# Performance work log

Measured on AMD Instinct MI355X. Metric: run time of the kernel, lower is better.

## Reference

```python
import jax, jax.numpy as jnp
import numpy as np

B, S, IN, OUT = 4, 2048, 4096, 16384

def setup_inputs() -> dict:
    key = jax.random.key(0)
    k1, k2, k3, k4 = jax.random.split(key, 4)
    x = jax.random.normal(k1, (B, S, IN), dtype=jnp.float32)
    quantized_weight = jax.random.randint(k2, (OUT, IN), 0, 16, dtype=jnp.int32)
    scale = jax.random.uniform(k3, (OUT,), dtype=jnp.float32)
    zero_point = jax.random.randint(k4, (OUT,), 0, 16, dtype=jnp.int32)
    return {"x": x, "quantized_weight": quantized_weight, "scale": scale, "zero_point": zero_point}

def reference(x, quantized_weight, scale, zero_point):
    # Per-output-channel dequantization: W = (q - zp) * scale, shape [OUT, IN]
    weight = (quantized_weight.astype(jnp.float32) - zero_point.astype(jnp.float32)[:, None]) * scale[:, None]
    # F.linear(x, W) = x @ W.T -> [B, S, OUT]
    return jnp.einsum('bsi,oi->bso', x, weight)
```

## Files before the change

kernel.cpp:

```cpp
#include <hip/hip_runtime.h>
#include <stdint.h>

#define MDIM 8192
#define NDIM 16384
#define KDIM 4096
#define NT   64

typedef __attribute__((ext_vector_type(4))) int i32x4;

__device__ __forceinline__ void gload_lds16(const void* g, void* l) {
    __builtin_amdgcn_global_load_lds(
        (const __attribute__((address_space(1))) void*)g,
        (__attribute__((address_space(3))) void*)l,
        16, 0, 0);
}

__device__ __forceinline__ i32x4 MFMA8(i32x4 a, i32x4 b, i32x4 c) {
    return __builtin_amdgcn_mfma_i32_16x16x64_i8(a, b, c, 0, 0, 0);
}


__global__ __launch_bounds__(256)
void quant_x_kernel(const float* __restrict__ x, int8_t* __restrict__ xq,
                    float* __restrict__ sx) {
    const int row = (int)blockIdx.x;
    const float* xr = x + (long)row * KDIM;
    const int t = threadIdx.x;
    float v[16];
#pragma unroll
    for (int i = 0; i < 4; ++i)
        *(float4*)&v[i * 4] = ((const float4*)xr)[t + 256 * i];
    float m = 0.f;
#pragma unroll
    for (int i = 0; i < 16; ++i) m = fmaxf(m, fabsf(v[i]));
#pragma unroll
    for (int off = 32; off >= 1; off >>= 1) m = fmaxf(m, __shfl_xor(m, off));
    __shared__ float red[4];
    if ((t & 63) == 0) red[t >> 6] = m;
    __syncthreads();
    m = fmaxf(fmaxf(red[0], red[1]), fmaxf(red[2], red[3]));
    m = fmaxf(m, 1e-20f);
    const float inv = 127.0f / m;
    if (t == 0) sx[row] = m * (1.0f / 127.0f);
    int* qo = (int*)(xq + (long)row * KDIM);
#pragma unroll
    for (int i = 0; i < 4; ++i) {
        union { int8_t c[4]; int w; } o;
#pragma unroll
        for (int j = 0; j < 4; ++j)
            o.c[j] = (int8_t)__float2int_rn(v[i * 4 + j] * inv);
        qo[t + 256 * i] = o.w;
    }
}

__global__ __launch_bounds__(256)
void quant_w_kernel(const int* __restrict__ q, const int* __restrict__ zp,
                    int8_t* __restrict__ wq) {
    const long i = (long)blockIdx.x * 256 + threadIdx.x;
    const long e = i * 16;
    const int o = (int)(e >> 12);
    const int z = zp[o];
    union { int8_t c[16]; int4 v; } r;
#pragma unroll
    for (int b = 0; b < 4; ++b) {
        int4 a = ((const int4*)(q + e))[b];
        r.c[b * 4 + 0] = (int8_t)(a.x - z);
        r.c[b * 4 + 1] = (int8_t)(a.y - z);
        r.c[b * 4 + 2] = (int8_t)(a.z - z);
        r.c[b * 4 + 3] = (int8_t)(a.w - z);
    }
    *(int4*)(wq + e) = r.v;
}


__global__ __launch_bounds__(512, 2)
void gemm_i8_kernel(const int8_t* __restrict__ A, const int8_t* __restrict__ Wt,
                    const float* __restrict__ scale, const float* __restrict__ sx,
                    float* __restrict__ C) {
    extern __shared__ int8_t lds[];

    const int wg = (int)blockIdx.x;
    const int rr = wg >> 8;
    const int ii = wg & 255;
    const int bm = ii & 31;
    const int bn = rr * 8 + (ii >> 5);

    const int tid  = threadIdx.x;
    const int lane = tid & 63;
    const int wid  = tid >> 6;
    const int wm   = wid >> 2;
    const int wn   = wid & 3;
    const int l15  = lane & 15;
    const int c16  = lane >> 4;

    const int axor = (l15 >> 1) & 3;
    const int fro  = l15 * 64 + ((c16 ^ axor) << 4);

    const int soff = (tid >> 2) * KDIM + ((((tid & 3) ^ ((tid >> 3) & 3))) << 4);
    const int dl   = tid * 16;

    const int8_t* Ab  = A  + (long)bm * 256 * KDIM;
    const int8_t* Wb  = Wt + (long)bn * 256 * KDIM;
    const int8_t* Ab2 = Ab + (long)128 * KDIM;
    const int8_t* Wb2 = Wb + (long)128 * KDIM;

#define STG(DSTB, SRC, TT) gload_lds16((SRC) + soff + (TT) * 64, &lds[(DSTB) + dl])

#define RDA4(DST, BB, IB)                                                           \
    _Pragma("unroll")                                                               \
    for (int i_ = 0; i_ < 4; ++i_)                                                  \
        DST[i_] = *(const i32x4*)&lds[(BB) + (wm * 128 + ((IB) + i_) * 16) * 64 + fro];

#define RDB2(DST, BB, JB)                                                           \
    _Pragma("unroll")                                                               \
    for (int j_ = 0; j_ < 2; ++j_)                                                  \
        DST[j_] = *(const i32x4*)&lds[(BB) + 16384 + (wn * 64 + ((JB) + j_) * 16) * 64 + fro];

#define MFQ(IB, JB, AS, BS)                                                         \
    do {                                                                            \
        __builtin_amdgcn_sched_barrier(0);                                          \
        __builtin_amdgcn_s_setprio(1);                                              \
        _Pragma("unroll")                                                           \
        for (int i_ = 0; i_ < 4; ++i_)                                              \
            _Pragma("unroll")                                                       \
            for (int j_ = 0; j_ < 2; ++j_)                                          \
                acc[(IB) + i_][(JB) + j_] =                                         \
                    MFMA8(AS[i_], BS[j_], acc[(IB) + i_][(JB) + j_]);               \
        __builtin_amdgcn_s_setprio(0);                                              \
        __builtin_amdgcn_sched_barrier(0);                                          \
    } while (0)

#define TILE(T, ACUR, BCUR, ANXT, BNXT)                                             \
    do {                                                                            \
             \
        RDA4(aHi, b0, 4);                                                           \
        asm volatile("s_waitcnt lgkmcnt(4)" ::: "memory");                          \
        MFQ(0, 0, ACUR, BCUR);                                                      \
                                                             \
        RDB2(bHi, b0, 2);                                                           \
        asm volatile("s_waitcnt lgkmcnt(2)" ::: "memory");                          \
        MFQ(4, 0, aHi, BCUR);                                                       \
                                        \
        if ((T) < NT - 1) {                                                         \
            RDA4(ANXT, b1, 0);                                                      \
            RDB2(BNXT, b1, 0);                                                      \
            asm volatile("s_waitcnt lgkmcnt(6)" ::: "memory");                      \
        } else {                                                                    \
            asm volatile("s_waitcnt lgkmcnt(0)" ::: "memory");                      \
        }                                                                           \
        MFQ(0, 2, ACUR, bHi);                                                       \
                    \
        {                                                                           \
            const int tt = ((T) + 3 < NT) ? ((T) + 3) : (NT - 1);                   \
            STG(b3 + 0, Ab, tt);  STG(b3 + 16384, Wb, tt);                          \
            STG(b3 + 8192, Ab2, tt); STG(b3 + 24576, Wb2, tt);                      \
        }                                                                           \
        asm volatile("s_waitcnt vmcnt(4)" ::: "memory");                            \
        __builtin_amdgcn_s_barrier();                                               \
        MFQ(4, 2, aHi, bHi);                                                        \
        { const int tb = b0; b0 = b1; b1 = b2; b2 = b3; b3 = tb; }                  \
    } while (0)

    i32x4 acc[8][4];
#pragma unroll
    for (int i = 0; i < 8; ++i)
#pragma unroll
        for (int j = 0; j < 4; ++j) acc[i][j] = (i32x4){0, 0, 0, 0};

    i32x4 aLoA[4], aLoB[4], aHi[4];
    i32x4 bLoA[2], bLoB[2], bHi[2];

    int b0 = 0, b1 = 32768, b2 = 65536, b3 = 98304;

    STG(b0 + 0, Ab, 0); STG(b0 + 16384, Wb, 0); STG(b0 + 8192, Ab2, 0); STG(b0 + 24576, Wb2, 0);
    STG(b1 + 0, Ab, 1); STG(b1 + 16384, Wb, 1); STG(b1 + 8192, Ab2, 1); STG(b1 + 24576, Wb2, 1);
    STG(b2 + 0, Ab, 2); STG(b2 + 16384, Wb, 2); STG(b2 + 8192, Ab2, 2); STG(b2 + 24576, Wb2, 2);
    asm volatile("s_waitcnt vmcnt(4)" ::: "memory");
    __builtin_amdgcn_s_barrier();
    RDA4(aLoA, b0, 0);
    RDB2(bLoA, b0, 0);

    for (int t = 0; t < NT; t += 2) {
        TILE(t,     aLoA, bLoA, aLoB, bLoB);
        TILE(t + 1, aLoB, bLoB, aLoA, bLoA);
    }
#undef TILE
#undef STG
#undef RDA4
#undef RDB2
#undef MFQ

    const long rowA0 = (long)bm * 256 + wm * 128;
    const int  colB0 = bn * 256 + wn * 64;
    float scj[4];
#pragma unroll
    for (int j = 0; j < 4; ++j) scj[j] = scale[colB0 + j * 16 + l15];
#pragma unroll
    for (int i = 0; i < 8; ++i) {
        const long rbase = rowA0 + i * 16 + c16 * 4;
        const float4 s4 = *(const float4*)(sx + rbase);
#pragma unroll
        for (int j = 0; j < 4; ++j) {
            float* cp = C + rbase * NDIM + colB0 + j * 16 + l15;
            cp[0 * (long)NDIM] = (float)acc[i][j][0] * scj[j] * s4.x;
            cp[1 * (long)NDIM] = (float)acc[i][j][1] * scj[j] * s4.y;
            cp[2 * (long)NDIM] = (float)acc[i][j][2] * scj[j] * s4.z;
            cp[3 * (long)NDIM] = (float)acc[i][j][3] * scj[j] * s4.w;
        }
    }
}


__global__ __launch_bounds__(256)
void fallback_kernel(const float* __restrict__ x, const int* __restrict__ q,
                     const float* __restrict__ scale, const int* __restrict__ zp,
                     float* __restrict__ out) {
    __shared__ float sA[64][17];
    __shared__ float sB[64][17];
    const int bn = (int)blockIdx.x % (NDIM / 64);
    const int bm = (int)blockIdx.x / (NDIM / 64);
    const int t  = threadIdx.x;
    const int tx = t & 15, ty = t >> 4;
    const long rowA = (long)bm * 64, rowB = (long)bn * 64;
    float acc[4][4] = {};
    for (int k0 = 0; k0 < KDIM; k0 += 16) {
#pragma unroll
        for (int i = 0; i < 4; ++i) {
            const int e = t + i * 256;
            const int r = e >> 4, c = e & 15;
            sA[r][c] = x[(rowA + r) * KDIM + k0 + c];
            const int o = (int)rowB + r;
            sB[r][c] = (float)(q[(long)o * KDIM + k0 + c] - zp[o]) * scale[o];
        }
        __syncthreads();
#pragma unroll
        for (int kk = 0; kk < 16; ++kk) {
            float a[4], b[4];
#pragma unroll
            for (int i = 0; i < 4; ++i) a[i] = sA[ty * 4 + i][kk];
#pragma unroll
            for (int j = 0; j < 4; ++j) b[j] = sB[tx * 4 + j][kk];
#pragma unroll
            for (int i = 0; i < 4; ++i)
#pragma unroll
                for (int j = 0; j < 4; ++j) acc[i][j] += a[i] * b[j];
        }
        __syncthreads();
    }
#pragma unroll
    for (int i = 0; i < 4; ++i) {
        const long r = rowA + ty * 4 + i;
#pragma unroll
        for (int j = 0; j < 4; ++j)
            out[r * NDIM + rowB + tx * 4 + j] = acc[i][j];
    }
}


extern "C" void kernel_launch(void* const* d_in, const int* in_sizes, int n_in,
                              void* d_out, int out_size, void* d_ws, size_t ws_size,
                              hipStream_t stream) {
    const float* x     = (const float*)d_in[0];
    const int*   qw    = (const int*)d_in[1];
    const float* scale = (const float*)d_in[2];
    const int*   zp    = (const int*)d_in[3];
    float*       out   = (float*)d_out;

    const size_t needA  = (size_t)MDIM * KDIM;
    const size_t needW  = (size_t)NDIM * KDIM;
    const size_t needSx = (size_t)MDIM * sizeof(float);

    if (ws_size >= needA + needW + needSx) {
        int8_t* xq = (int8_t*)d_ws;
        int8_t* wq = xq + needA;
        float*  sx = (float*)((char*)d_ws + needA + needW);
        quant_x_kernel<<<MDIM, 256, 0, stream>>>(x, xq, sx);
        quant_w_kernel<<<(NDIM * (KDIM / 16)) / 256, 256, 0, stream>>>(qw, zp, wq);
        (void)hipFuncSetAttribute((const void*)gemm_i8_kernel,
                                  hipFuncAttributeMaxDynamicSharedMemorySize, 131072);
        gemm_i8_kernel<<<(MDIM / 256) * (NDIM / 256), 512, 131072, stream>>>(xq, wq, scale, sx, out);
    } else {
        fallback_kernel<<<(MDIM / 64) * (NDIM / 64), 256, 0, stream>>>(x, qw, scale, zp, out);
    }
}
```

Measured before the change: 700.9 us.

## Prefetch whole next-tile fragments into registers and issue all MFMAs in one block

Measured after the change: 705.4 us. About the same (+0.6%).

```diff
diff --git a/kernel.cpp b/kernel.cpp
--- a/kernel.cpp
+++ b/kernel.cpp
@@ -106,58 +106,46 @@
 
 #define STG(DSTB, SRC, TT) gload_lds16((SRC) + soff + (TT) * 64, &lds[(DSTB) + dl])
 
-#define RDA4(DST, BB, IB)                                                           \
+#define RDA8(DST, BB)                                                               \
     _Pragma("unroll")                                                               \
-    for (int i_ = 0; i_ < 4; ++i_)                                                  \
-        DST[i_] = *(const i32x4*)&lds[(BB) + (wm * 128 + ((IB) + i_) * 16) * 64 + fro];
-
-#define RDB2(DST, BB, JB)                                                           \
+    for (int i_ = 0; i_ < 8; ++i_)                                                  \
+        DST[i_] = *(const i32x4*)&lds[(BB) + (wm * 128 + i_ * 16) * 64 + fro];
+
+#define RDB4(DST, BB)                                                               \
     _Pragma("unroll")                                                               \
-    for (int j_ = 0; j_ < 2; ++j_)                                                  \
-        DST[j_] = *(const i32x4*)&lds[(BB) + 16384 + (wn * 64 + ((JB) + j_) * 16) * 64 + fro];
-
-#define MFQ(IB, JB, AS, BS)                                                         \
+    for (int j_ = 0; j_ < 4; ++j_)                                                  \
+        DST[j_] = *(const i32x4*)&lds[(BB) + 16384 + (wn * 64 + j_ * 16) * 64 + fro];
+
+#define MFMAALL(AS, BS)                                                             \
     do {                                                                            \
         __builtin_amdgcn_sched_barrier(0);                                          \
         __builtin_amdgcn_s_setprio(1);                                              \
         _Pragma("unroll")                                                           \
-        for (int i_ = 0; i_ < 4; ++i_)                                              \
+        for (int i_ = 0; i_ < 8; ++i_)                                              \
             _Pragma("unroll")                                                       \
-            for (int j_ = 0; j_ < 2; ++j_)                                          \
-                acc[(IB) + i_][(JB) + j_] =                                         \
-                    MFMA8(AS[i_], BS[j_], acc[(IB) + i_][(JB) + j_]);               \
+            for (int j_ = 0; j_ < 4; ++j_)                                          \
+                acc[i_][j_] = MFMA8(AS[i_], BS[j_], acc[i_][j_]);                   \
         __builtin_amdgcn_s_setprio(0);                                              \
         __builtin_amdgcn_sched_barrier(0);                                          \
     } while (0)
 
-#define TILE(T, ACUR, BCUR, ANXT, BNXT)                                             \
+#define TILE(T, CA, CB, NA, NB)                                                     \
     do {                                                                            \
-             \
-        RDA4(aHi, b0, 4);                                                           \
-        asm volatile("s_waitcnt lgkmcnt(4)" ::: "memory");                          \
-        MFQ(0, 0, ACUR, BCUR);                                                      \
-                                                             \
-        RDB2(bHi, b0, 2);                                                           \
-        asm volatile("s_waitcnt lgkmcnt(2)" ::: "memory");                          \
-        MFQ(4, 0, aHi, BCUR);                                                       \
-                                        \
         if ((T) < NT - 1) {                                                         \
-            RDA4(ANXT, b1, 0);                                                      \
-            RDB2(BNXT, b1, 0);                                                      \
-            asm volatile("s_waitcnt lgkmcnt(6)" ::: "memory");                      \
+            RDA8(NA, b1);                                                           \
+            RDB4(NB, b1);                                                           \
+            asm volatile("s_waitcnt lgkmcnt(12)" ::: "memory");                     \
         } else {                                                                    \
             asm volatile("s_waitcnt lgkmcnt(0)" ::: "memory");                      \
         }                                                                           \
-        MFQ(0, 2, ACUR, bHi);                                                       \
-                    \
         {                                                                           \
             const int tt = ((T) + 3 < NT) ? ((T) + 3) : (NT - 1);                   \
             STG(b3 + 0, Ab, tt);  STG(b3 + 16384, Wb, tt);                          \
             STG(b3 + 8192, Ab2, tt); STG(b3 + 24576, Wb2, tt);                      \
         }                                                                           \
+        MFMAALL(CA, CB);                                                            \
         asm volatile("s_waitcnt vmcnt(4)" ::: "memory");                            \
         __builtin_amdgcn_s_barrier();                                               \
-        MFQ(4, 2, aHi, bHi);                                                        \
         { const int tb = b0; b0 = b1; b1 = b2; b2 = b3; b3 = tb; }                  \
     } while (0)
 
@@ -167,8 +155,8 @@
 #pragma unroll
         for (int j = 0; j < 4; ++j) acc[i][j] = (i32x4){0, 0, 0, 0};
 
-    i32x4 aLoA[4], aLoB[4], aHi[4];
-    i32x4 bLoA[2], bLoB[2], bHi[2];
+    i32x4 aA[8], aB[8];
+    i32x4 bA[4], bB[4];
 
     int b0 = 0, b1 = 32768, b2 = 65536, b3 = 98304;
 
@@ -177,18 +165,18 @@
     STG(b2 + 0, Ab, 2); STG(b2 + 16384, Wb, 2); STG(b2 + 8192, Ab2, 2); STG(b2 + 24576, Wb2, 2);
     asm volatile("s_waitcnt vmcnt(4)" ::: "memory");
     __builtin_amdgcn_s_barrier();
-    RDA4(aLoA, b0, 0);
-    RDB2(bLoA, b0, 0);
+    RDA8(aA, b0);
+    RDB4(bA, b0);
 
     for (int t = 0; t < NT; t += 2) {
-        TILE(t,     aLoA, bLoA, aLoB, bLoB);
-        TILE(t + 1, aLoB, bLoB, aLoA, bLoA);
+        TILE(t,     aA, bA, aB, bB);
+        TILE(t + 1, aB, bB, aA, bA);
     }
 #undef TILE
 #undef STG
-#undef RDA4
-#undef RDB2
-#undef MFQ
+#undef RDA8
+#undef RDB4
+#undef MFMAALL
 
     const long rowA0 = (long)bm * 256 + wm * 128;
     const int  colB0 = bn * 256 + wn * 64;
```
